# Optimization experiments

Measured on AMD Instinct MI355X. Metric: run time of the kernel, lower is better.

Reference implementation:

```python
import jax, jax.numpy as jnp
import numpy as np

D = 1024
H = 16
B = 8
N = 1024


def setup_inputs() -> dict:
    key = jax.random.key(0)
    k1, k2, k3 = jax.random.split(key, 3)
    x = jax.random.normal(k1, (B, N, D), dtype=jnp.float32)
    w_in = jax.random.normal(k2, (D, 3 * D), dtype=jnp.float32) * (1.0 / np.sqrt(D))
    w_out = jax.random.normal(k3, (D, D), dtype=jnp.float32) * (1.0 / np.sqrt(D))
    b_out = jnp.zeros((D,), dtype=jnp.float32)
    return {"x": x, "w_in": w_in, "w_out": w_out, "b_out": b_out}


def reference(x, w_in, w_out, b_out):
    h = H
    d = D // H
    scale = D ** (-0.5)  # note: full dimension, per source
    qkv = x @ w_in  # [B, N, 3D]
    # rearrange 'b n (qkv h d) -> qkv b h n d'
    qkv = qkv.reshape(x.shape[0], x.shape[1], 3, h, d)
    qkv = jnp.transpose(qkv, (2, 0, 3, 1, 4))
    q, k, v = qkv[0], qkv[1], qkv[2]
    scores = jnp.einsum('bhid,bhjd->bhij', q, k) * scale
    attn = jax.nn.softmax(scores, axis=-1)
    out = jnp.einsum('bhij,bhjd->bhid', attn, v)
    # 'b h n d -> b n (h d)'
    out = jnp.transpose(out, (0, 2, 1, 3)).reshape(x.shape[0], x.shape[1], h * d)
    return out @ w_out + b_out
```

## Files before the change

kernel.cpp:

```cpp
#include <hip/hip_runtime.h>
#include <stdint.h>
#include <stddef.h>

typedef __bf16 bf16;
typedef __bf16 bf16x4 __attribute__((ext_vector_type(4)));
typedef __bf16 bf16x8 __attribute__((ext_vector_type(8)));
typedef float  f32x4  __attribute__((ext_vector_type(4)));
typedef float  f32x16 __attribute__((ext_vector_type(16)));
typedef float  f32x4v __attribute__((ext_vector_type(4)));

__device__ __forceinline__ void gload_lds16(const void* g, void* lds) {
  __builtin_amdgcn_global_load_lds(
      (__attribute__((address_space(1))) void*)(uintptr_t)g,
      (__attribute__((address_space(3))) void*)lds,
      16, 0, 0);
}


__global__ void cvt_f32_to_bf16(const float* __restrict__ in, bf16* __restrict__ out, int n) {
  int i = (blockIdx.x * blockDim.x + threadIdx.x) * 4;
  if (i >= n) return;
  f32x4v v = *reinterpret_cast<const f32x4v*>(in + i);
  bf16x4 o;
  o[0] = (bf16)v[0]; o[1] = (bf16)v[1]; o[2] = (bf16)v[2]; o[3] = (bf16)v[3];
  *reinterpret_cast<bf16x4*>(out + i) = o;
}

__global__ void transpose_cvt(const float* __restrict__ in, bf16* __restrict__ out, int R, int C) {
  __shared__ bf16 tile[32][33];
  int c0 = blockIdx.x * 32, r0 = blockIdx.y * 32;
  int tx = threadIdx.x, ty = threadIdx.y;
  #pragma unroll
  for (int i = ty; i < 32; i += 8)
    tile[i][tx] = (bf16)in[(size_t)(r0 + i) * C + (c0 + tx)];
  __syncthreads();
  #pragma unroll
  for (int i = ty; i < 32; i += 8)
    out[(size_t)(c0 + i) * R + (r0 + tx)] = tile[tx][i];
}


template <typename OT, bool BIAS>
__global__ __launch_bounds__(256) void gemm_abt(
    const bf16* __restrict__ A,
    const bf16* __restrict__ Bt,
    const float* __restrict__ bias,
    OT* __restrict__ C, int M, int N, int K)
{
  __shared__ bf16 As[128 * 64];
  __shared__ bf16 Bs[128 * 64];

  const int tid = threadIdx.x;
  const int w = tid >> 6, l = tid & 63;
  const int l15 = l & 15, l4 = l >> 4, l7 = l & 7;
  const int wr = w >> 1, wc = w & 1;
  const int m0 = blockIdx.y * 128, n0 = blockIdx.x * 128;

  f32x4 acc[4][4];
  #pragma unroll
  for (int i = 0; i < 4; i++)
    #pragma unroll
    for (int j = 0; j < 4; j++) acc[i][j] = (f32x4){0.f, 0.f, 0.f, 0.f};

  const int srow  = w * 8 + (l >> 3);
  const int sslot = (l & 7) ^ ((l >> 3) & 7);
  const int KT = K >> 6;

  for (int kt = 0; kt < KT; ++kt) {
    __syncthreads();
    const int kcol = kt * 64 + sslot * 8;
    #pragma unroll
    for (int p = 0; p < 4; ++p) {
      gload_lds16(A  + (size_t)(m0 + p * 32 + srow) * K + kcol,
                  (char*)As + p * 4096 + w * 1024);
      gload_lds16(Bt + (size_t)(n0 + p * 32 + srow) * K + kcol,
                  (char*)Bs + p * 4096 + w * 1024);
    }
    __syncthreads();

    #pragma unroll
    for (int kk = 0; kk < 2; ++kk) {
      const int coff = (kk * 32 + l4 * 8) ^ (l7 << 3);
      bf16x8 af[4], bq[4];
      #pragma unroll
      for (int m = 0; m < 4; ++m) {
        int r = wr * 64 + m * 16 + l15;
        af[m] = *reinterpret_cast<const bf16x8*>(&As[r * 64 + coff]);
      }
      #pragma unroll
      for (int n = 0; n < 4; ++n) {
        int r = wc * 64 + n * 16 + l15;
        bq[n] = *reinterpret_cast<const bf16x8*>(&Bs[r * 64 + coff]);
      }
      #pragma unroll
      for (int m = 0; m < 4; ++m)
        #pragma unroll
        for (int n = 0; n < 4; ++n)
          acc[m][n] = __builtin_amdgcn_mfma_f32_16x16x32_bf16(af[m], bq[n], acc[m][n], 0, 0, 0);
    }
  }

  #pragma unroll
  for (int m = 0; m < 4; ++m) {
    #pragma unroll
    for (int n = 0; n < 4; ++n) {
      int col = n0 + wc * 64 + n * 16 + l15;
      float bv = BIAS ? bias[col] : 0.f;
      #pragma unroll
      for (int j = 0; j < 4; ++j) {
        int row = m0 + wr * 64 + m * 16 + l4 * 4 + j;
        float v = acc[m][n][j] + bv;
        C[(size_t)row * N + col] = (OT)v;
      }
    }
  }
}


__global__ __launch_bounds__(256) void attn_fused(
    const bf16* __restrict__ qkv,
    bf16* __restrict__ aout)
{
  __shared__ bf16 Ks[64 * 64];
  __shared__ bf16 Vt[64 * 64];
  __shared__ bf16 Pl[4][32 * 64];

  const int tid = threadIdx.x;
  const int w = tid >> 6, l = tid & 63;
  const int l31 = l & 31, hi = l >> 5;

  const int bid = blockIdx.x;
  const int c  = bid & 7, rr = bid >> 3;
  const int g  = c * 16 + (rr & 15);
  const int qt = rr >> 4;
  const int h  = g & 15;
  const int b  = g >> 4;

  const bf16* base = qkv + (size_t)b * 1024 * 3072;
  const int qrow0 = qt * 128 + w * 32;

  const float qscale = 0.03125f * 1.44269504f;
  bf16x8 qf[4];
  #pragma unroll
  for (int st = 0; st < 4; st++) {
    const bf16* p = base + (size_t)(qrow0 + l31) * 3072 + h * 64 + st * 16 + hi * 8;
    bf16x8 v = *reinterpret_cast<const bf16x8*>(p);
    #pragma unroll
    for (int e = 0; e < 8; e++) v[e] = (bf16)((float)v[e] * qscale);
    qf[st] = v;
  }

  f32x16 acc0 = {}, acc1 = {};
  float lsum = 0.f;

  const int skey  = w * 8 + (l >> 3);
  const int sslot = (l & 7) ^ ((l >> 3) & 7);
  const int vd0   = (tid & 15) * 4;
  const int vk0   = (tid >> 4) * 4;
  const int vslot = tid >> 5;
  const int vhalf = (tid >> 4) & 1;

  for (int kt = 0; kt < 16; ++kt) {
    __syncthreads();
    #pragma unroll
    for (int p = 0; p < 2; ++p)
      gload_lds16(base + (size_t)(kt * 64 + p * 32 + skey) * 3072 + 1024 + h * 64 + sslot * 8,
                  (char*)Ks + p * 4096 + w * 1024);
    {
      bf16x4 vv[4];
      #pragma unroll
      for (int i = 0; i < 4; ++i)
        vv[i] = *reinterpret_cast<const bf16x4*>(
            base + (size_t)(kt * 64 + vk0 + i) * 3072 + 2048 + h * 64 + vd0);
      #pragma unroll
      for (int j = 0; j < 4; ++j) {
        int d = vd0 + j;
        bf16x4 o; o[0] = vv[0][j]; o[1] = vv[1][j]; o[2] = vv[2][j]; o[3] = vv[3][j];
        *reinterpret_cast<bf16x4*>(&Vt[d * 64 + ((vslot ^ (d & 7)) * 8 + vhalf * 4)]) = o;
      }
    }
    __syncthreads();

    #pragma unroll
    for (int ktile = 0; ktile < 2; ++ktile) {
      f32x16 s = {};
      const int key = ktile * 32 + l31;
      #pragma unroll
      for (int st = 0; st < 4; ++st) {
        const int slot = (2 * st + hi) ^ (key & 7);
        bf16x8 kf = *reinterpret_cast<const bf16x8*>(&Ks[key * 64 + slot * 8]);
        s = __builtin_amdgcn_mfma_f32_32x32x16_bf16(kf, qf[st], s, 0, 0, 0);
      }
      #pragma unroll
      for (int gq = 0; gq < 4; ++gq) {
        bf16x4 pb;
        #pragma unroll
        for (int j2 = 0; j2 < 4; ++j2) {
          float pv = exp2f(s[4 * gq + j2]);
          lsum += pv;
          pb[j2] = (bf16)pv;
        }
        const int chunk = ktile * 4 + gq;
        *reinterpret_cast<bf16x4*>(
            &Pl[w][l31 * 64 + ((chunk ^ (l31 & 7)) * 8 + hi * 4)]) = pb;
      }
    }

    #pragma unroll
    for (int st = 0; st < 4; ++st) {
      const int cslot = (2 * st + hi) ^ (l31 & 7);
      bf16x8 pa  = *reinterpret_cast<const bf16x8*>(&Pl[w][l31 * 64 + cslot * 8]);
      bf16x8 vf0 = *reinterpret_cast<const bf16x8*>(&Vt[l31 * 64 + cslot * 8]);
      acc0 = __builtin_amdgcn_mfma_f32_32x32x16_bf16(pa, vf0, acc0, 0, 0, 0);
      bf16x8 vf1 = *reinterpret_cast<const bf16x8*>(&Vt[(32 + l31) * 64 + cslot * 8]);
      acc1 = __builtin_amdgcn_mfma_f32_32x32x16_bf16(pa, vf1, acc1, 0, 0, 0);
    }
  }

  float tf = lsum + __shfl_xor(lsum, 32);

  #pragma unroll
  for (int reg = 0; reg < 16; ++reg) {
    int q_r = (reg & 3) + 8 * (reg >> 2) + 4 * hi;
    float rinv = 1.0f / __shfl(tf, q_r);
    size_t rowoff = ((size_t)b * 1024 + qrow0 + q_r) * 1024 + h * 64;
    aout[rowoff + l31]      = (bf16)(acc0[reg] * rinv);
    aout[rowoff + 32 + l31] = (bf16)(acc1[reg] * rinv);
  }
}


extern "C" void kernel_launch(void* const* d_in, const int* in_sizes, int n_in,
                              void* d_out, int out_size, void* d_ws, size_t ws_size,
                              hipStream_t stream) {
  const float* x     = (const float*)d_in[0];
  const float* w_in  = (const float*)d_in[1];
  const float* w_out = (const float*)d_in[2];
  const float* b_out = (const float*)d_in[3];
  float* out = (float*)d_out;

  bf16* xb    = (bf16*)d_ws;
  bf16* wint  = xb    + (size_t)8192 * 1024;
  bf16* woutt = wint  + (size_t)3072 * 1024;
  bf16* qkv   = woutt + (size_t)1024 * 1024;
  bf16* ao    = qkv   + (size_t)8192 * 3072;

  cvt_f32_to_bf16<<<8192, 256, 0, stream>>>(x, xb, 8192 * 1024);
  transpose_cvt<<<dim3(96, 32), dim3(32, 8), 0, stream>>>(w_in,  wint,  1024, 3072);
  transpose_cvt<<<dim3(32, 32), dim3(32, 8), 0, stream>>>(w_out, woutt, 1024, 1024);

  gemm_abt<bf16, false><<<dim3(24, 64), 256, 0, stream>>>(xb, wint, nullptr, qkv, 8192, 3072, 1024);

  attn_fused<<<1024, 256, 0, stream>>>(qkv, ao);

  gemm_abt<float, true><<<dim3(8, 64), 256, 0, stream>>>(ao, woutt, b_out, out, 8192, 1024, 1024);
}
```

Before: 186.2 us.

## Keep softmax probabilities in registers and compute row sums via MFMA

Removes the per-wave LDS staging buffer for probabilities: the exp'd scores from the S=K·Q MFMA output are packed directly into bf16 operand registers and fed to the P·V MFMA, with V fragments gathered from two half-slots to match the register layout. Row sums are accumulated by an extra MFMA against a ones vector instead of scalar adds plus shuffles. This saves LDS writes/reads and a shuffle reduction but adds two MFMAs per key tile, extra V reads, and sums computed from bf16-rounded probabilities.

```diff
diff --git a/kernel.cpp b/kernel.cpp
--- a/kernel.cpp
+++ b/kernel.cpp
@@ -8,12 +8,19 @@
 typedef float  f32x4  __attribute__((ext_vector_type(4)));
 typedef float  f32x16 __attribute__((ext_vector_type(16)));
 typedef float  f32x4v __attribute__((ext_vector_type(4)));
+typedef unsigned int u32x4 __attribute__((ext_vector_type(4)));
 
 __device__ __forceinline__ void gload_lds16(const void* g, void* lds) {
   __builtin_amdgcn_global_load_lds(
       (__attribute__((address_space(1))) void*)(uintptr_t)g,
       (__attribute__((address_space(3))) void*)lds,
       16, 0, 0);
+}
+
+__device__ __forceinline__ unsigned int pk2(float a, float b) {
+  unsigned short lo = __builtin_bit_cast(unsigned short, (bf16)a);
+  unsigned short hi = __builtin_bit_cast(unsigned short, (bf16)b);
+  return (unsigned int)lo | ((unsigned int)hi << 16);
 }
 
 
@@ -123,7 +130,6 @@
 {
   __shared__ bf16 Ks[64 * 64];
   __shared__ bf16 Vt[64 * 64];
-  __shared__ bf16 Pl[4][32 * 64];
 
   const int tid = threadIdx.x;
   const int w = tid >> 6, l = tid & 63;
@@ -150,8 +156,11 @@
     qf[st] = v;
   }
 
-  f32x16 acc0 = {}, acc1 = {};
-  float lsum = 0.f;
+  bf16x8 onesf;
+  #pragma unroll
+  for (int e = 0; e < 8; e++) onesf[e] = (bf16)1.0f;
+
+  f32x16 acc0 = {}, acc1 = {}, accS = {};
 
   const int skey  = w * 8 + (l >> 3);
   const int sslot = (l & 7) ^ ((l >> 3) & 7);
@@ -192,37 +201,47 @@
         s = __builtin_amdgcn_mfma_f32_32x32x16_bf16(kf, qf[st], s, 0, 0, 0);
       }
       #pragma unroll
-      for (int gq = 0; gq < 4; ++gq) {
-        bf16x4 pb;
+      for (int r = 0; r < 16; ++r) s[r] = exp2f(s[r]);
+      u32x4 dw0 = {pk2(s[0], s[1]),  pk2(s[2], s[3]),
+                   pk2(s[4], s[5]),  pk2(s[6], s[7])};
+      u32x4 dw1 = {pk2(s[8], s[9]),  pk2(s[10], s[11]),
+                   pk2(s[12], s[13]), pk2(s[14], s[15])};
+      bf16x8 pf0 = __builtin_bit_cast(bf16x8, dw0);
+      bf16x8 pf1 = __builtin_bit_cast(bf16x8, dw1);
+
+      accS = __builtin_amdgcn_mfma_f32_32x32x16_bf16(pf0, onesf, accS, 0, 0, 0);
+      accS = __builtin_amdgcn_mfma_f32_32x32x16_bf16(pf1, onesf, accS, 0, 0, 0);
+
+      #pragma unroll
+      for (int gg = 0; gg < 2; ++gg) {
+        bf16x8 pf = gg ? pf1 : pf0;
+        const int cb = ktile * 4 + gg * 2;
+        const int d7 = l31 & 7;
+        bf16x4 a0 = *reinterpret_cast<const bf16x4*>(
+            &Vt[l31 * 64 + ((cb ^ d7) * 8 + hi * 4)]);
+        bf16x4 b0 = *reinterpret_cast<const bf16x4*>(
+            &Vt[l31 * 64 + (((cb + 1) ^ d7) * 8 + hi * 4)]);
+        bf16x8 vf0;
         #pragma unroll
-        for (int j2 = 0; j2 < 4; ++j2) {
-          float pv = exp2f(s[4 * gq + j2]);
-          lsum += pv;
-          pb[j2] = (bf16)pv;
-        }
-        const int chunk = ktile * 4 + gq;
-        *reinterpret_cast<bf16x4*>(
-            &Pl[w][l31 * 64 + ((chunk ^ (l31 & 7)) * 8 + hi * 4)]) = pb;
-      }
-    }
-
-    #pragma unroll
-    for (int st = 0; st < 4; ++st) {
-      const int cslot = (2 * st + hi) ^ (l31 & 7);
-      bf16x8 pa  = *reinterpret_cast<const bf16x8*>(&Pl[w][l31 * 64 + cslot * 8]);
-      bf16x8 vf0 = *reinterpret_cast<const bf16x8*>(&Vt[l31 * 64 + cslot * 8]);
-      acc0 = __builtin_amdgcn_mfma_f32_32x32x16_bf16(pa, vf0, acc0, 0, 0, 0);
-      bf16x8 vf1 = *reinterpret_cast<const bf16x8*>(&Vt[(32 + l31) * 64 + cslot * 8]);
-      acc1 = __builtin_amdgcn_mfma_f32_32x32x16_bf16(pa, vf1, acc1, 0, 0, 0);
-    }
-  }
-
-  float tf = lsum + __shfl_xor(lsum, 32);
+        for (int e = 0; e < 4; ++e) { vf0[e] = a0[e]; vf0[4 + e] = b0[e]; }
+        acc0 = __builtin_amdgcn_mfma_f32_32x32x16_bf16(pf, vf0, acc0, 0, 0, 0);
+
+        bf16x4 a1 = *reinterpret_cast<const bf16x4*>(
+            &Vt[(32 + l31) * 64 + ((cb ^ d7) * 8 + hi * 4)]);
+        bf16x4 b1 = *reinterpret_cast<const bf16x4*>(
+            &Vt[(32 + l31) * 64 + (((cb + 1) ^ d7) * 8 + hi * 4)]);
+        bf16x8 vf1;
+        #pragma unroll
+        for (int e = 0; e < 4; ++e) { vf1[e] = a1[e]; vf1[4 + e] = b1[e]; }
+        acc1 = __builtin_amdgcn_mfma_f32_32x32x16_bf16(pf, vf1, acc1, 0, 0, 0);
+      }
+    }
+  }
 
   #pragma unroll
   for (int reg = 0; reg < 16; ++reg) {
     int q_r = (reg & 3) + 8 * (reg >> 2) + 4 * hi;
-    float rinv = 1.0f / __shfl(tf, q_r);
+    float rinv = 1.0f / accS[reg];
     size_t rowoff = ((size_t)b * 1024 + qrow0 + q_r) * 1024 + h * 64;
     aout[rowoff + l31]      = (bf16)(acc0[reg] * rinv);
     aout[rowoff + 32 + l31] = (bf16)(acc1[reg] * rinv);
```

Result: no change. 188.8 us (+1.4%).
